# Kernel optimization log

Hardware: AMD Instinct MI355X
Metric: run time of the kernel (lower is better)

Reference implementation:

```python
import jax, jax.numpy as jnp
import numpy as np

B, S, D_IN, D_OUT = 4, 2048, 4096, 4096
SPARSE_FRACTION = 0.9


def setup_inputs() -> dict:
    key = jax.random.key(0)
    k_x, k_w, k_m = jax.random.split(key, 3)
    x = jax.random.normal(k_x, (B, S, D_IN), dtype=jnp.float32)
    # kaiming_uniform_(a=sqrt(5)) -> U(-bound, bound), bound = sqrt(6/((1+a^2)*fan_in)) = 1/sqrt(fan_in)
    bound = 1.0 / np.sqrt(D_IN)
    weight = jax.random.uniform(k_w, (D_OUT, D_IN), dtype=jnp.float32,
                                minval=-bound, maxval=bound)
    # mask: exactly (1 - sparse_fraction) of entries are True (random permutation)
    num_params = D_OUT * D_IN
    num_sparse = int(num_params * SPARSE_FRACTION)
    perm = jax.random.permutation(k_m, num_params)
    mask_flat = jnp.ones((num_params,), dtype=jnp.float32).at[perm[:num_sparse]].set(0.0)
    mask = mask_flat.reshape(D_OUT, D_IN).astype(jnp.bool_)
    return {"x": x, "weight": weight, "mask": mask}


def reference(x, weight, mask):
    # masked_weight = weight * mask; out = x @ masked_weight.T
    masked_weight = weight * mask.astype(weight.dtype)  # [out, in]
    return jnp.einsum('bsi,oi->bso', x, masked_weight)
```

## Files before the change

### kernel.cpp

```cpp
#include <hip/hip_runtime.h>
#include <stdint.h>


static constexpr int Mdim = 8192;
static constexpr int Ndim = 4096;
static constexpr int Kdim = 4096;
static constexpr int BM = 128;
static constexpr int BN = 128;
static constexpr int BK = 64;

typedef __attribute__((ext_vector_type(8))) short short8;
typedef __attribute__((ext_vector_type(4))) float float4v;
typedef __attribute__((ext_vector_type(16))) float float16v;
typedef __attribute__((ext_vector_type(4))) int int4v;
typedef __attribute__((ext_vector_type(8))) unsigned short ushort8;

__device__ __forceinline__ unsigned short f32_to_bf16(float f) {
  union { float f; uint32_t u; } c; c.f = f;
  uint32_t u = c.u;
  u += 0x7fffu + ((u >> 16) & 1u);
  return (unsigned short)(u >> 16);
}

__global__ void detect_mask_kernel(const unsigned char* __restrict__ m, int* __restrict__ flag) {
  int found = 0;
  const int total = 1 << 20;
  for (int p = blockIdx.x * blockDim.x + threadIdx.x; p < total;
       p += gridDim.x * blockDim.x)
    found |= (m[4 * p + 1] != 0);
  if (__any(found) && (threadIdx.x & 63) == 0) atomicOr(flag, 1);
}

__global__ void cvt_x_kernel(const float* __restrict__ x, unsigned short* __restrict__ o) {
  long i = (blockIdx.x * (long)blockDim.x + threadIdx.x) * 8;
  float4v v0 = *(const float4v*)(x + i);
  float4v v1 = *(const float4v*)(x + i + 4);
  ushort8 r;
  r[0] = f32_to_bf16(v0[0]); r[1] = f32_to_bf16(v0[1]);
  r[2] = f32_to_bf16(v0[2]); r[3] = f32_to_bf16(v0[3]);
  r[4] = f32_to_bf16(v1[0]); r[5] = f32_to_bf16(v1[1]);
  r[6] = f32_to_bf16(v1[2]); r[7] = f32_to_bf16(v1[3]);
  *(ushort8*)(o + i) = r;
}

__global__ void cvt_w_kernel(const float* __restrict__ w, const unsigned char* __restrict__ mraw,
                             const int* __restrict__ flag, unsigned short* __restrict__ o) {
  long i = (blockIdx.x * (long)blockDim.x + threadIdx.x) * 8;
  float4v w0 = *(const float4v*)(w + i);
  float4v w1 = *(const float4v*)(w + i + 4);
  int m[8];
  if (*flag) {
    unsigned long long mb = *(const unsigned long long*)(mraw + i);
#pragma unroll
    for (int j = 0; j < 8; ++j) m[j] = ((mb >> (8 * j)) & 0xffull) != 0;
  } else {
    int4v a = *(const int4v*)((const int*)mraw + i);
    int4v b = *(const int4v*)((const int*)mraw + i + 4);
#pragma unroll
    for (int j = 0; j < 4; ++j) { m[j] = a[j] != 0; m[4 + j] = b[j] != 0; }
  }
  ushort8 r;
  r[0] = f32_to_bf16(m[0] ? w0[0] : 0.0f);
  r[1] = f32_to_bf16(m[1] ? w0[1] : 0.0f);
  r[2] = f32_to_bf16(m[2] ? w0[2] : 0.0f);
  r[3] = f32_to_bf16(m[3] ? w0[3] : 0.0f);
  r[4] = f32_to_bf16(m[4] ? w1[0] : 0.0f);
  r[5] = f32_to_bf16(m[5] ? w1[1] : 0.0f);
  r[6] = f32_to_bf16(m[6] ? w1[2] : 0.0f);
  r[7] = f32_to_bf16(m[7] ? w1[3] : 0.0f);
  *(ushort8*)(o + i) = r;
}

__global__ __launch_bounds__(256) void gemm_bt_kernel(const unsigned short* __restrict__ X,
                                                      const unsigned short* __restrict__ W,
                                                      float* __restrict__ O) {
  __shared__ short sA[BM * BK];
  __shared__ short sB[BN * BK];

  const int tid = threadIdx.x;
  const int lane = tid & 63;
  const int wave = tid >> 6;
  const int wr = wave >> 1;
  const int wc = wave & 1;

  const int bid = blockIdx.x;
  const int grp512 = bid >> 9;
  const int rres = bid & 511;
  const int tm = (grp512 << 4) | (rres & 15);
  const int tn = rres >> 4;
  const int row0 = tm * BM;
  const int col0 = tn * BN;

  float16v acc[2][2];
#pragma unroll
  for (int i = 0; i < 2; ++i)
#pragma unroll
    for (int j = 0; j < 2; ++j)
#pragma unroll
      for (int r = 0; r < 16; ++r) acc[i][j][r] = 0.f;

  int srow[4], scol[4];
#pragma unroll
  for (int r = 0; r < 4; ++r) {
    int c = r * 256 + tid;
    srow[r] = c >> 3;
    scol[r] = (((c & 7) ^ (srow[r] & 7)) * 8);
  }

  const int ml = lane & 31;
  const int kg = lane >> 5;
  const int sw = lane & 7;

  for (int kt = 0; kt < Kdim; kt += BK) {
#pragma unroll
    for (int r = 0; r < 4; ++r) {
      const unsigned short* gA = X + (long)(row0 + srow[r]) * Kdim + kt + scol[r];
      const unsigned short* gB = W + (long)(col0 + srow[r]) * Kdim + kt + scol[r];
      const int loff = (r * 256 + tid) * 16;
      __builtin_amdgcn_global_load_lds((const __attribute__((address_space(1))) void*)gA,
                                       (__attribute__((address_space(3))) void*)((char*)sA + loff),
                                       16, 0, 0);
      __builtin_amdgcn_global_load_lds((const __attribute__((address_space(1))) void*)gB,
                                       (__attribute__((address_space(3))) void*)((char*)sB + loff),
                                       16, 0, 0);
    }
    __syncthreads();

#pragma unroll
    for (int s = 0; s < 4; ++s) {
      const int pos = ((((s << 1) | kg) ^ sw) << 3);
      short8 a[2], b[2];
#pragma unroll
      for (int i = 0; i < 2; ++i)
        a[i] = *(const short8*)(sA + (wr * 64 + i * 32 + ml) * BK + pos);
#pragma unroll
      for (int j = 0; j < 2; ++j)
        b[j] = *(const short8*)(sB + (wc * 64 + j * 32 + ml) * BK + pos);
#pragma unroll
      for (int i = 0; i < 2; ++i)
#pragma unroll
        for (int j = 0; j < 2; ++j)
          acc[i][j] = __builtin_amdgcn_mfma_f32_32x32x16_bf16(a[i], b[j], acc[i][j], 0, 0, 0);
    }
    __syncthreads();
  }

#pragma unroll
  for (int i = 0; i < 2; ++i) {
#pragma unroll
    for (int j = 0; j < 2; ++j) {
      const long rbase = row0 + wr * 64 + i * 32;
      const long cg = col0 + wc * 64 + j * 32 + ml;
#pragma unroll
      for (int reg = 0; reg < 16; ++reg) {
        const long row = rbase + (reg & 3) + 8 * (reg >> 2) + 4 * kg;
        O[row * (long)Ndim + cg] = acc[i][j][reg];
      }
    }
  }
}

__global__ void gemm_fallback_kernel(const float* __restrict__ X, const float* __restrict__ Wt,
                                     const unsigned char* __restrict__ mraw,
                                     const int* __restrict__ flag, float* __restrict__ O) {
  __shared__ float sX[16][17];
  __shared__ float sW[16][17];
  const int tx = threadIdx.x & 15;
  const int ty = threadIdx.x >> 4;
  const long row = blockIdx.y * 16 + ty;
  const long colblock = blockIdx.x * 16;
  const int byteLayout = *flag;
  float acc = 0.f;
  for (int k0 = 0; k0 < Kdim; k0 += 16) {
    sX[ty][tx] = X[row * Kdim + k0 + tx];
    const long wi = (colblock + ty) * (long)Kdim + k0 + tx;
    const int mv = byteLayout ? (mraw[wi] != 0) : (((const int*)mraw)[wi] != 0);
    sW[ty][tx] = mv ? Wt[wi] : 0.f;
    __syncthreads();
#pragma unroll
    for (int k = 0; k < 16; ++k) acc += sX[ty][k] * sW[tx][k];
    __syncthreads();
  }
  O[row * Ndim + colblock + tx] = acc;
}

extern "C" void kernel_launch(void* const* d_in, const int* in_sizes, int n_in,
                              void* d_out, int out_size, void* d_ws, size_t ws_size,
                              hipStream_t stream) {
  const float* x = (const float*)d_in[0];
  const float* w = (const float*)d_in[1];
  const unsigned char* mask = (const unsigned char*)d_in[2];
  float* out = (float*)d_out;

  const size_t xb_off = 0;
  const size_t wb_off = (size_t)Mdim * Kdim * 2;
  const size_t flag_off = wb_off + (size_t)Ndim * Kdim * 2;
  const size_t needed = flag_off + 16;

  if (ws_size >= needed) {
    unsigned short* xb = (unsigned short*)((char*)d_ws + xb_off);
    unsigned short* wb = (unsigned short*)((char*)d_ws + wb_off);
    int* flag = (int*)((char*)d_ws + flag_off);

    hipMemsetAsync(flag, 0, sizeof(int), stream);
    detect_mask_kernel<<<64, 256, 0, stream>>>(mask, flag);
    cvt_x_kernel<<<(int)(((long)Mdim * Kdim / 8) / 256), 256, 0, stream>>>(x, xb);
    cvt_w_kernel<<<(int)(((long)Ndim * Kdim / 8) / 256), 256, 0, stream>>>(w, mask, flag, wb);
    gemm_bt_kernel<<<(Mdim / BM) * (Ndim / BN), 256, 0, stream>>>(xb, wb, out);
  } else {
    int* flag = (int*)d_ws;
    hipMemsetAsync(flag, 0, sizeof(int), stream);
    detect_mask_kernel<<<64, 256, 0, stream>>>(mask, flag);
    dim3 grid(Ndim / 16, Mdim / 16);
    gemm_fallback_kernel<<<grid, 256, 0, stream>>>(x, w, mask, flag, out);
  }
}
```

Measured before the change: 611.2 us.

## Rewrite bf16 GEMM as 256x256 tile, 8-wave, software-pipelined MFMA kernel

Replaces the 128x128 single-buffered GEMM with a 256x256 tile using 512 threads, 16x16x32 MFMAs and a 128KB LDS double-buffered ring. Global-to-LDS loads for the next K tiles are interleaved with MFMA phases using explicit barriers, waitcnt, sched_barrier and setprio, so memory transfer overlaps compute. The aim is higher arithmetic intensity per tile and hidden load latency. In exchange it uses large LDS and many registers, which limits occupancy, and the hand-tuned waitcnt accounting is fragile. It also changes the block-to-tile mapping for L2 locality.

```diff
diff --git a/kernel.cpp b/kernel.cpp
--- a/kernel.cpp
+++ b/kernel.cpp
@@ -5,13 +5,14 @@
 static constexpr int Mdim = 8192;
 static constexpr int Ndim = 4096;
 static constexpr int Kdim = 4096;
-static constexpr int BM = 128;
-static constexpr int BN = 128;
+static constexpr int BM = 256;
+static constexpr int BN = 256;
 static constexpr int BK = 64;
+static constexpr int NT = Kdim / BK;
 
 typedef __attribute__((ext_vector_type(8))) short short8;
 typedef __attribute__((ext_vector_type(4))) float float4v;
-typedef __attribute__((ext_vector_type(16))) float float16v;
+typedef __attribute__((ext_vector_type(4))) float f32x4;
 typedef __attribute__((ext_vector_type(4))) int int4v;
 typedef __attribute__((ext_vector_type(8))) unsigned short ushort8;
 
@@ -71,93 +72,171 @@
   *(ushort8*)(o + i) = r;
 }
 
-__global__ __launch_bounds__(256) void gemm_bt_kernel(const unsigned short* __restrict__ X,
-                                                      const unsigned short* __restrict__ W,
-                                                      float* __restrict__ O) {
-  __shared__ short sA[BM * BK];
-  __shared__ short sB[BN * BK];
+
+__device__ __forceinline__ void stage_half(const unsigned short* __restrict__ src,
+                                           int grow_base, int kelem, char* region,
+                                           int r0, int l0, int gcol) {
+  const unsigned short* g0 = src + (size_t)(grow_base + r0) * Kdim + kelem + gcol;
+  const unsigned short* g1 = src + (size_t)(grow_base + r0 + 8) * Kdim + kelem + gcol;
+  __builtin_amdgcn_global_load_lds((const __attribute__((address_space(1))) void*)g0,
+                                   (__attribute__((address_space(3))) void*)(region + l0),
+                                   16, 0, 0);
+  __builtin_amdgcn_global_load_lds((const __attribute__((address_space(1))) void*)g1,
+                                   (__attribute__((address_space(3))) void*)(region + l0 + 1024),
+                                   16, 0, 0);
+}
+
+template <int BUF, int MI0>
+__device__ __forceinline__ void load_a(short8 (&a)[4][2], const char* sA,
+                                       int wm, int arow, int kg, int w7) {
+#pragma unroll
+  for (int mi = 0; mi < 4; ++mi) {
+    const char* rowp = sA + (BUF * 2 + wm) * 16384 + ((MI0 + mi) * 16 + arow) * 128;
+#pragma unroll
+    for (int s = 0; s < 2; ++s)
+      a[mi][s] = *(const short8*)(rowp + (((s << 2) | kg) ^ w7) * 16);
+  }
+}
+
+template <int BUF, int NI0>
+__device__ __forceinline__ void load_b(short8 (&b)[4][2], const char* sB,
+                                       int wnh, int brow, int kg, int w7) {
+#pragma unroll
+  for (int ni = 0; ni < 2; ++ni) {
+    const char* rowp = sB + (BUF * 2 + wnh) * 16384 + (brow + (NI0 + ni) * 16) * 128;
+#pragma unroll
+    for (int s = 0; s < 2; ++s)
+      b[NI0 + ni][s] = *(const short8*)(rowp + (((s << 2) | kg) ^ w7) * 16);
+  }
+}
+
+template <int MIB, int NIB>
+__device__ __forceinline__ void mfma_quad(f32x4 (&acc)[8][4], const short8 (&a)[4][2],
+                                          const short8 (&b)[4][2]) {
+#pragma unroll
+  for (int s = 0; s < 2; ++s)
+#pragma unroll
+    for (int mi = 0; mi < 4; ++mi)
+#pragma unroll
+      for (int ni = 0; ni < 2; ++ni)
+        acc[MIB + mi][NIB + ni] = __builtin_amdgcn_mfma_f32_16x16x32_bf16(
+            a[mi][s], b[NIB + ni][s], acc[MIB + mi][NIB + ni], 0, 0, 0);
+}
+
+__device__ __forceinline__ void phase_pre() {
+  __builtin_amdgcn_sched_barrier(0);
+  __builtin_amdgcn_s_barrier();
+  asm volatile("s_waitcnt lgkmcnt(0)" ::: "memory");
+  __builtin_amdgcn_sched_barrier(0);
+  __builtin_amdgcn_s_setprio(1);
+}
+
+__device__ __forceinline__ void phase_post() {
+  __builtin_amdgcn_s_setprio(0);
+  __builtin_amdgcn_sched_barrier(0);
+  __builtin_amdgcn_s_barrier();
+}
+
+__device__ __forceinline__ void phase_post_vm() {
+  __builtin_amdgcn_s_setprio(0);
+  __builtin_amdgcn_sched_barrier(0);
+  asm volatile("s_waitcnt vmcnt(4)" ::: "memory");
+  __builtin_amdgcn_sched_barrier(0);
+  __builtin_amdgcn_s_barrier();
+}
+
+__global__ __launch_bounds__(512, 2) void gemm_bt_kernel(const unsigned short* __restrict__ X,
+                                                         const unsigned short* __restrict__ W,
+                                                         float* __restrict__ O) {
+  __shared__ __align__(16) char lds[131072];
+  char* sA = lds;
+  char* sB = lds + 65536;
 
   const int tid = threadIdx.x;
   const int lane = tid & 63;
   const int wave = tid >> 6;
-  const int wr = wave >> 1;
-  const int wc = wave & 1;
+  const int wm = wave >> 2;
+  const int wn = wave & 3;
+  const int wnh = wn >> 1;
 
   const int bid = blockIdx.x;
-  const int grp512 = bid >> 9;
-  const int rres = bid & 511;
-  const int tm = (grp512 << 4) | (rres & 15);
-  const int tn = rres >> 4;
+  const int id = (bid & 7) * 64 + (bid >> 3);
+  const int tm = id >> 4;
+  const int tn = id & 15;
   const int row0 = tm * BM;
   const int col0 = tn * BN;
 
-  float16v acc[2][2];
-#pragma unroll
-  for (int i = 0; i < 2; ++i)
-#pragma unroll
-    for (int j = 0; j < 2; ++j)
-#pragma unroll
-      for (int r = 0; r < 16; ++r) acc[i][j][r] = 0.f;
-
-  int srow[4], scol[4];
-#pragma unroll
-  for (int r = 0; r < 4; ++r) {
-    int c = r * 256 + tid;
-    srow[r] = c >> 3;
-    scol[r] = (((c & 7) ^ (srow[r] & 7)) * 8);
-  }
-
-  const int ml = lane & 31;
-  const int kg = lane >> 5;
-  const int sw = lane & 7;
-
-  for (int kt = 0; kt < Kdim; kt += BK) {
-#pragma unroll
-    for (int r = 0; r < 4; ++r) {
-      const unsigned short* gA = X + (long)(row0 + srow[r]) * Kdim + kt + scol[r];
-      const unsigned short* gB = W + (long)(col0 + srow[r]) * Kdim + kt + scol[r];
-      const int loff = (r * 256 + tid) * 16;
-      __builtin_amdgcn_global_load_lds((const __attribute__((address_space(1))) void*)gA,
-                                       (__attribute__((address_space(3))) void*)((char*)sA + loff),
-                                       16, 0, 0);
-      __builtin_amdgcn_global_load_lds((const __attribute__((address_space(1))) void*)gB,
-                                       (__attribute__((address_space(3))) void*)((char*)sB + loff),
-                                       16, 0, 0);
-    }
-    __syncthreads();
-
-#pragma unroll
-    for (int s = 0; s < 4; ++s) {
-      const int pos = ((((s << 1) | kg) ^ sw) << 3);
-      short8 a[2], b[2];
-#pragma unroll
-      for (int i = 0; i < 2; ++i)
-        a[i] = *(const short8*)(sA + (wr * 64 + i * 32 + ml) * BK + pos);
-#pragma unroll
-      for (int j = 0; j < 2; ++j)
-        b[j] = *(const short8*)(sB + (wc * 64 + j * 32 + ml) * BK + pos);
-#pragma unroll
-      for (int i = 0; i < 2; ++i)
-#pragma unroll
-        for (int j = 0; j < 2; ++j)
-          acc[i][j] = __builtin_amdgcn_mfma_f32_32x32x16_bf16(a[i], b[j], acc[i][j], 0, 0, 0);
-    }
-    __syncthreads();
-  }
-
-#pragma unroll
-  for (int i = 0; i < 2; ++i) {
-#pragma unroll
-    for (int j = 0; j < 2; ++j) {
-      const long rbase = row0 + wr * 64 + i * 32;
-      const long cg = col0 + wc * 64 + j * 32 + ml;
-#pragma unroll
-      for (int reg = 0; reg < 16; ++reg) {
-        const long row = rbase + (reg & 3) + 8 * (reg >> 2) + 4 * kg;
-        O[row * (long)Ndim + cg] = acc[i][j][reg];
-      }
-    }
-  }
+  const int r0 = wave * 16 + (lane >> 3);
+  const int gcol = ((lane & 7) ^ (lane >> 3)) * 8;
+  const int l0 = wave * 2048 + lane * 16;
+
+  const int arow = lane & 15;
+  const int kg = lane >> 4;
+  const int w7 = lane & 7;
+  const int brow = (wn & 1) * 64 + arow;
+
+  f32x4 acc[8][4];
+#pragma unroll
+  for (int i = 0; i < 8; ++i)
+#pragma unroll
+    for (int j = 0; j < 4; ++j)
+#pragma unroll
+      for (int r = 0; r < 4; ++r) acc[i][j][r] = 0.f;
+
+  short8 a[4][2], b[4][2];
+
+  stage_half(X, row0 + 0,   0 * BK, sA + 0 * 16384, r0, l0, gcol);
+  stage_half(X, row0 + 128, 0 * BK, sA + 1 * 16384, r0, l0, gcol);
+  stage_half(W, col0 + 0,   0 * BK, sB + 0 * 16384, r0, l0, gcol);
+  stage_half(W, col0 + 128, 0 * BK, sB + 1 * 16384, r0, l0, gcol);
+  stage_half(W, col0 + 0,   1 * BK, sB + 2 * 16384, r0, l0, gcol);
+  stage_half(W, col0 + 128, 1 * BK, sB + 3 * 16384, r0, l0, gcol);
+  asm volatile("s_waitcnt vmcnt(4)" ::: "memory");
+  __builtin_amdgcn_sched_barrier(0);
+  __builtin_amdgcn_s_barrier();
+
+#pragma unroll 1
+  for (int it = 0; it < NT / 2; ++it) {
+    const int t1 = 2 * it + 1;
+    const int t2 = (2 * it + 2) & (NT - 1);
+    const int t3 = (2 * it + 3) & (NT - 1);
+
+    load_a<0, 0>(a, sA, wm, arow, kg, w7);
+    load_b<0, 0>(b, sB, wnh, brow, kg, w7);
+    stage_half(X, row0 + 0, t1 * BK, sA + 2 * 16384, r0, l0, gcol);
+    phase_pre(); mfma_quad<0, 0>(acc, a, b); phase_post();
+    load_b<0, 2>(b, sB, wnh, brow, kg, w7);
+    stage_half(X, row0 + 128, t1 * BK, sA + 3 * 16384, r0, l0, gcol);
+    phase_pre(); mfma_quad<0, 2>(acc, a, b); phase_post();
+    load_a<0, 4>(a, sA, wm, arow, kg, w7);
+    stage_half(W, col0 + 0, t2 * BK, sB + 0 * 16384, r0, l0, gcol);
+    phase_pre(); mfma_quad<4, 0>(acc, a, b); phase_post();
+    stage_half(W, col0 + 128, t2 * BK, sB + 1 * 16384, r0, l0, gcol);
+    phase_pre(); mfma_quad<4, 2>(acc, a, b); phase_post_vm();
+
+    load_a<1, 0>(a, sA, wm, arow, kg, w7);
+    load_b<1, 0>(b, sB, wnh, brow, kg, w7);
+    stage_half(X, row0 + 0, t2 * BK, sA + 0 * 16384, r0, l0, gcol);
+    phase_pre(); mfma_quad<0, 0>(acc, a, b); phase_post();
+    load_b<1, 2>(b, sB, wnh, brow, kg, w7);
+    stage_half(X, row0 + 128, t2 * BK, sA + 1 * 16384, r0, l0, gcol);
+    phase_pre(); mfma_quad<0, 2>(acc, a, b); phase_post();
+    load_a<1, 4>(a, sA, wm, arow, kg, w7);
+    stage_half(W, col0 + 0, t3 * BK, sB + 2 * 16384, r0, l0, gcol);
+    phase_pre(); mfma_quad<4, 0>(acc, a, b); phase_post();
+    stage_half(W, col0 + 128, t3 * BK, sB + 3 * 16384, r0, l0, gcol);
+    phase_pre(); mfma_quad<4, 2>(acc, a, b); phase_post_vm();
+  }
+
+  const int orow0 = row0 + wm * 128 + kg * 4;
+  const int ocol0 = col0 + wn * 64 + arow;
+#pragma unroll
+  for (int mi = 0; mi < 8; ++mi)
+#pragma unroll
+    for (int ni = 0; ni < 4; ++ni)
+#pragma unroll
+      for (int r = 0; r < 4; ++r)
+        O[(size_t)(orow0 + mi * 16 + r) * Ndim + ocol0 + ni * 16] = acc[mi][ni][r];
 }
 
 __global__ void gemm_fallback_kernel(const float* __restrict__ X, const float* __restrict__ Wt,
@@ -206,7 +285,7 @@
     detect_mask_kernel<<<64, 256, 0, stream>>>(mask, flag);
     cvt_x_kernel<<<(int)(((long)Mdim * Kdim / 8) / 256), 256, 0, stream>>>(x, xb);
     cvt_w_kernel<<<(int)(((long)Ndim * Kdim / 8) / 256), 256, 0, stream>>>(w, mask, flag, wb);
-    gemm_bt_kernel<<<(Mdim / BM) * (Ndim / BN), 256, 0, stream>>>(xb, wb, out);
+    gemm_bt_kernel<<<(Mdim / BM) * (Ndim / BN), 512, 0, stream>>>(xb, wb, out);
   } else {
     int* flag = (int*)d_ws;
     hipMemsetAsync(flag, 0, sizeof(int), stream);
```

Result: faster. 537.5 us (-12.1%).

## Rewrite bf16 GEMM with triple-buffered LDS pipeline and 256x128 tiles

Applied to the files above, without the earlier changes.

Replaces the single-buffered 128x128x64 GEMM with a 256x128x32 tile run by 512 threads (8 waves). Global-to-LDS loads go into a three-stage ring buffer so loads for step t+2 overlap MFMA work on step t, with s_setprio and split barriers around the compute phases. It also switches to 16x16x32 MFMA instructions and remaps block IDs for L2 locality. The cost is a 72KB LDS footprint that limits occupancy, plus partial vmcnt waits whose correctness depends on the exact count of outstanding loads.

```diff
diff --git a/kernel.cpp b/kernel.cpp
--- a/kernel.cpp
+++ b/kernel.cpp
@@ -5,13 +5,14 @@
 static constexpr int Mdim = 8192;
 static constexpr int Ndim = 4096;
 static constexpr int Kdim = 4096;
-static constexpr int BM = 128;
+static constexpr int BM = 256;
 static constexpr int BN = 128;
-static constexpr int BK = 64;
+static constexpr int BK = 32;
+static constexpr int NT = Kdim / BK;
 
 typedef __attribute__((ext_vector_type(8))) short short8;
 typedef __attribute__((ext_vector_type(4))) float float4v;
-typedef __attribute__((ext_vector_type(16))) float float16v;
+typedef __attribute__((ext_vector_type(4))) float f32x4;
 typedef __attribute__((ext_vector_type(4))) int int4v;
 typedef __attribute__((ext_vector_type(8))) unsigned short ushort8;
 
@@ -71,93 +72,130 @@
   *(ushort8*)(o + i) = r;
 }
 
-__global__ __launch_bounds__(256) void gemm_bt_kernel(const unsigned short* __restrict__ X,
-                                                      const unsigned short* __restrict__ W,
-                                                      float* __restrict__ O) {
-  __shared__ short sA[BM * BK];
-  __shared__ short sB[BN * BK];
+
+__device__ __forceinline__ void gload16(const unsigned short* g, char* l) {
+  __builtin_amdgcn_global_load_lds((const __attribute__((address_space(1))) void*)g,
+                                   (__attribute__((address_space(3))) void*)l, 16, 0, 0);
+}
+
+__device__ __forceinline__ void phase_pre() {
+  __builtin_amdgcn_s_barrier();
+  __builtin_amdgcn_s_setprio(1);
+}
+
+__device__ __forceinline__ void phase_post() {
+  __builtin_amdgcn_s_setprio(0);
+  __builtin_amdgcn_s_barrier();
+}
+
+__device__ __forceinline__ void phase_post_vm() {
+  __builtin_amdgcn_s_setprio(0);
+  asm volatile("s_waitcnt vmcnt(3)" ::: "memory");
+  __builtin_amdgcn_s_barrier();
+}
+
+__global__ __launch_bounds__(512, 4) void gemm_bt_kernel(const unsigned short* __restrict__ X,
+                                                         const unsigned short* __restrict__ W,
+                                                         float* __restrict__ O) {
+  __shared__ __align__(16) char lds[73728];
+  char* sA = lds;
+  char* sB = lds + 49152;
 
   const int tid = threadIdx.x;
   const int lane = tid & 63;
   const int wave = tid >> 6;
-  const int wr = wave >> 1;
-  const int wc = wave & 1;
+  const int wm = wave >> 1;
+  const int wn = wave & 1;
 
   const int bid = blockIdx.x;
-  const int grp512 = bid >> 9;
-  const int rres = bid & 511;
-  const int tm = (grp512 << 4) | (rres & 15);
-  const int tn = rres >> 4;
+  const int id = (bid & 7) * 128 + (bid >> 3);
+  const int tm = id >> 5;
+  const int tn = id & 31;
   const int row0 = tm * BM;
   const int col0 = tn * BN;
 
-  float16v acc[2][2];
-#pragma unroll
-  for (int i = 0; i < 2; ++i)
-#pragma unroll
-    for (int j = 0; j < 2; ++j)
-#pragma unroll
-      for (int r = 0; r < 16; ++r) acc[i][j][r] = 0.f;
-
-  int srow[4], scol[4];
-#pragma unroll
-  for (int r = 0; r < 4; ++r) {
-    int c = r * 256 + tid;
-    srow[r] = c >> 3;
-    scol[r] = (((c & 7) ^ (srow[r] & 7)) * 8);
-  }
-
-  const int ml = lane & 31;
-  const int kg = lane >> 5;
-  const int sw = lane & 7;
-
-  for (int kt = 0; kt < Kdim; kt += BK) {
-#pragma unroll
-    for (int r = 0; r < 4; ++r) {
-      const unsigned short* gA = X + (long)(row0 + srow[r]) * Kdim + kt + scol[r];
-      const unsigned short* gB = W + (long)(col0 + srow[r]) * Kdim + kt + scol[r];
-      const int loff = (r * 256 + tid) * 16;
-      __builtin_amdgcn_global_load_lds((const __attribute__((address_space(1))) void*)gA,
-                                       (__attribute__((address_space(3))) void*)((char*)sA + loff),
-                                       16, 0, 0);
-      __builtin_amdgcn_global_load_lds((const __attribute__((address_space(1))) void*)gB,
-                                       (__attribute__((address_space(3))) void*)((char*)sB + loff),
-                                       16, 0, 0);
-    }
-    __syncthreads();
-
-#pragma unroll
-    for (int s = 0; s < 4; ++s) {
-      const int pos = ((((s << 1) | kg) ^ sw) << 3);
-      short8 a[2], b[2];
-#pragma unroll
-      for (int i = 0; i < 2; ++i)
-        a[i] = *(const short8*)(sA + (wr * 64 + i * 32 + ml) * BK + pos);
-#pragma unroll
-      for (int j = 0; j < 2; ++j)
-        b[j] = *(const short8*)(sB + (wc * 64 + j * 32 + ml) * BK + pos);
-#pragma unroll
-      for (int i = 0; i < 2; ++i)
-#pragma unroll
-        for (int j = 0; j < 2; ++j)
-          acc[i][j] = __builtin_amdgcn_mfma_f32_32x32x16_bf16(a[i], b[j], acc[i][j], 0, 0, 0);
-    }
-    __syncthreads();
-  }
-
-#pragma unroll
-  for (int i = 0; i < 2; ++i) {
-#pragma unroll
-    for (int j = 0; j < 2; ++j) {
-      const long rbase = row0 + wr * 64 + i * 32;
-      const long cg = col0 + wc * 64 + j * 32 + ml;
-#pragma unroll
-      for (int reg = 0; reg < 16; ++reg) {
-        const long row = rbase + (reg & 3) + 8 * (reg >> 2) + 4 * kg;
-        O[row * (long)Ndim + cg] = acc[i][j][reg];
-      }
-    }
-  }
+  const int sr = tid >> 2;
+  const int sc = ((tid & 3) ^ (sr & 3)) * 8;
+  const int l0 = tid * 16;
+
+  const unsigned short* gA = X + (size_t)(row0 + sr) * Kdim + sc;
+  const unsigned short* gB = W + (size_t)(col0 + sr) * Kdim + sc;
+
+  const int arow = lane & 15;
+  const int kg = lane >> 4;
+  const int cb = (kg ^ (lane & 3)) * 16;
+  const int abase = (wm * 64 + arow) * 64 + cb;
+  const int bbase = (wn * 64 + arow) * 64 + cb;
+
+  f32x4 acc[4][4];
+#pragma unroll
+  for (int i = 0; i < 4; ++i)
+#pragma unroll
+    for (int j = 0; j < 4; ++j)
+#pragma unroll
+      for (int r = 0; r < 4; ++r) acc[i][j][r] = 0.f;
+
+  short8 a[4], b[4];
+
+  gload16(gA, sA + l0);
+  gload16(gA + (size_t)128 * Kdim, sA + 8192 + l0);
+  gload16(gB, sB + l0);
+  gload16(gA + BK, sA + 16384 + l0);
+  gload16(gA + (size_t)128 * Kdim + BK, sA + 24576 + l0);
+  gload16(gB + BK, sB + 8192 + l0);
+  asm volatile("s_waitcnt vmcnt(3)" ::: "memory");
+  __builtin_amdgcn_s_barrier();
+
+  int rc = 0;
+#pragma unroll 1
+  for (int t = 0; t < NT; ++t) {
+    const int sb = (rc == 0) ? 2 : rc - 1;
+    const int ks = ((t + 2) & (NT - 1)) * BK;
+    const char* pA = sA + rc * 16384;
+    const char* pB = sB + rc * 8192;
+    char* qA = sA + sb * 16384;
+    char* qB = sB + sb * 8192;
+
+#pragma unroll
+    for (int mi = 0; mi < 4; ++mi)
+      a[mi] = *(const short8*)(pA + abase + mi * 1024);
+#pragma unroll
+    for (int ni = 0; ni < 2; ++ni)
+      b[ni] = *(const short8*)(pB + bbase + ni * 1024);
+    gload16(gA + ks, qA + l0);
+    gload16(gA + (size_t)128 * Kdim + ks, qA + 8192 + l0);
+    phase_pre();
+#pragma unroll
+    for (int mi = 0; mi < 4; ++mi)
+#pragma unroll
+      for (int ni = 0; ni < 2; ++ni)
+        acc[mi][ni] = __builtin_amdgcn_mfma_f32_16x16x32_bf16(a[mi], b[ni], acc[mi][ni], 0, 0, 0);
+    phase_post();
+
+#pragma unroll
+    for (int ni = 2; ni < 4; ++ni)
+      b[ni] = *(const short8*)(pB + bbase + ni * 1024);
+    gload16(gB + ks, qB + l0);
+    phase_pre();
+#pragma unroll
+    for (int mi = 0; mi < 4; ++mi)
+#pragma unroll
+      for (int ni = 2; ni < 4; ++ni)
+        acc[mi][ni] = __builtin_amdgcn_mfma_f32_16x16x32_bf16(a[mi], b[ni], acc[mi][ni], 0, 0, 0);
+    phase_post_vm();
+
+    rc = (rc == 2) ? 0 : rc + 1;
+  }
+
+  const int orow0 = row0 + wm * 64 + kg * 4;
+  const int ocol0 = col0 + wn * 64 + arow;
+#pragma unroll
+  for (int mi = 0; mi < 4; ++mi)
+#pragma unroll
+    for (int ni = 0; ni < 4; ++ni)
+#pragma unroll
+      for (int r = 0; r < 4; ++r)
+        O[(size_t)(orow0 + mi * 16 + r) * Ndim + ocol0 + ni * 16] = acc[mi][ni][r];
 }
 
 __global__ void gemm_fallback_kernel(const float* __restrict__ X, const float* __restrict__ Wt,
@@ -206,7 +244,7 @@
     detect_mask_kernel<<<64, 256, 0, stream>>>(mask, flag);
     cvt_x_kernel<<<(int)(((long)Mdim * Kdim / 8) / 256), 256, 0, stream>>>(x, xb);
     cvt_w_kernel<<<(int)(((long)Ndim * Kdim / 8) / 256), 256, 0, stream>>>(w, mask, flag, wb);
-    gemm_bt_kernel<<<(Mdim / BM) * (Ndim / BN), 256, 0, stream>>>(xb, wb, out);
+    gemm_bt_kernel<<<(Mdim / BM) * (Ndim / BN), 512, 0, stream>>>(xb, wb, out);
   } else {
     int* flag = (int*)d_ws;
     hipMemsetAsync(flag, 0, sizeof(int), stream);
```

Result: no change. 608.8 us (-0.4%).
